# Kernel tuning notes

Hardware: AMD Instinct MI355X
Metric: run time of the kernel (lower is better)

The kernel has to match this reference:

```python
import jax, jax.numpy as jnp
import numpy as np

PATCH = 8
C1 = 1e-4
C2 = 1e-3
EPS = 1e-3
ALPHA = 0.4
WEIGHTS = (1.0, 0.01, 1.0)


def charbonnier(x):
    return (x * x + EPS * EPS) ** ALPHA


def resize_bilinear_ac(img, H2, W2):
    # bilinear resize with align_corners=True (matches F.interpolate)
    B, C, H, W = img.shape
    fy = jnp.arange(H2, dtype=img.dtype) * ((H - 1) / max(H2 - 1, 1))
    fx = jnp.arange(W2, dtype=img.dtype) * ((W - 1) / max(W2 - 1, 1))
    y0 = jnp.clip(jnp.floor(fy).astype(jnp.int32), 0, H - 2)
    x0 = jnp.clip(jnp.floor(fx).astype(jnp.int32), 0, W - 2)
    wy = (fy - y0)[None, None, :, None]
    wx = (fx - x0)[None, None, None, :]
    rows = img[:, :, y0, :] * (1 - wy) + img[:, :, y0 + 1, :] * wy  # [B,C,H2,W]
    out = rows[:, :, :, x0] * (1 - wx) + rows[:, :, :, x0 + 1] * wx  # [B,C,H2,W2]
    return out


def bilinear_warp(img, flow):
    # backward warp: sample img at (x + u, y + v), bilinear, border clamp
    B, C, H, W = img.shape
    gx = jnp.arange(W, dtype=img.dtype)[None, None, :] + flow[:, 0]  # [B,H,W]
    gy = jnp.arange(H, dtype=img.dtype)[None, :, None] + flow[:, 1]  # [B,H,W]
    x0f = jnp.floor(gx)
    y0f = jnp.floor(gy)
    wx = (gx - x0f)[:, None]  # [B,1,H,W]
    wy = (gy - y0f)[:, None]
    x0 = jnp.clip(x0f.astype(jnp.int32), 0, W - 1)
    x1 = jnp.clip(x0 + 1, 0, W - 1)
    y0 = jnp.clip(y0f.astype(jnp.int32), 0, H - 1)
    y1 = jnp.clip(y0 + 1, 0, H - 1)
    imgf = img.reshape(B, C, H * W)

    def gather(yi, xi):
        idx = (yi * W + xi).reshape(B, 1, H * W)
        g = jnp.take_along_axis(imgf, jnp.broadcast_to(idx, (B, C, H * W)), axis=2)
        return g.reshape(B, C, H, W)

    v00 = gather(y0, x0)
    v01 = gather(y0, x1)
    v10 = gather(y1, x0)
    v11 = gather(y1, x1)
    top = v00 * (1 - wx) + v01 * wx
    bot = v10 * (1 - wx) + v11 * wx
    return top * (1 - wy) + bot * wy


def torch_gradient(x, axis):
    # torch.gradient: central diff interior, one-sided at edges, spacing 1
    n = x.shape[axis]
    sl = lambda a, b: jax.lax.slice_in_dim(x, a, b, axis=axis)
    first = sl(1, 2) - sl(0, 1)
    interior = (sl(2, n) - sl(0, n - 2)) * 0.5
    last = sl(n - 1, n) - sl(n - 2, n - 1)
    return jnp.concatenate([first, interior, last], axis=axis)


def ssim_score(I1, I2):
    # faithful to SSIMLoss: stats pooled over ALL non-overlapping patches per
    # (batch, channel), i.e. over the region cropped to multiples of patch.
    B, C, H, W = I1.shape
    p = min(PATCH, H)
    PH, PW = H // p, W // p
    x = I1[:, :, :PH * p, :PW * p].reshape(B, C, -1)
    y = I2[:, :, :PH * p, :PW * p].reshape(B, C, -1)
    N = x.shape[-1]
    mu1 = x.mean(-1)
    mu2 = y.mean(-1)
    d1 = x - mu1[..., None]
    d2 = y - mu2[..., None]
    var1 = (d1 * d1).sum(-1) / (N - 1)  # torch .var() is unbiased
    var2 = (d2 * d2).sum(-1) / (N - 1)
    s12 = (d1 * d2).mean(-1)
    num = (2 * mu1 * mu2 + C1) * (2 * s12 + C2)
    den = (mu1 ** 2 + mu2 ** 2 + C1) * (var1 + var2 + C2)
    return num / den  # [B, C]


def setup_inputs() -> dict:
    key = jax.random.key(0)
    k1, k2 = jax.random.split(key)
    images = jax.random.uniform(k1, (16, 33, 256, 256), dtype=jnp.float32)
    flows = jax.random.normal(k2, (16, 20, 128, 128), dtype=jnp.float32)
    return {"images": images, "flows": flows}


def reference(images, flows):
    B, Cf, FH, FW = flows.shape
    n_flows = Cf // 2  # 10 frame pairs
    imgs = resize_bilinear_ac(images, FH, FW)  # [B,33,FH,FW]
    src = imgs[:, 3:].reshape(B * n_flows, 3, FH, FW)
    fl = flows.reshape(B * n_flows, 2, FH, FW)
    warped = bilinear_warp(src, fl).reshape(B, n_flows * 3, FH, FW)
    ref = imgs[:, : n_flows * 3]

    similarity_loss = ssim_score(ref, warped).mean()

    flow_x = flows[:, 0::2]
    flow_y = flows[:, 1::2]
    smooth = (charbonnier(torch_gradient(flow_x, 1))
              + charbonnier(torch_gradient(flow_x, 2))
              + charbonnier(torch_gradient(flow_y, 1))
              + charbonnier(torch_gradient(flow_y, 2))).mean()

    pixel_loss = charbonnier(ref - warped).mean()

    return WEIGHTS[0] * pixel_loss + WEIGHTS[1] * smooth + WEIGHTS[2] * similarity_loss
```

## Files before the change

kernel.cpp:

```cpp
#include <hip/hip_runtime.h>

#define IH 256
#define IW 256
#define FH 128
#define FW 128
#define NB 16
#define ICH 33
#define NF 10
#define NC 30
#define PL (FH * FW)
#define SPLIT 8
#define ROWS_PP (FH / SPLIT)
#define LOSS_BLOCKS (NB * NC * SPLIT)
#define SMOOTH_BLOCKS 480
#define HALO 5
#define SROWS (ROWS_PP + 2 * HALO + 1)
#define PART_STRIDE 8

__device__ __forceinline__ float charb(float g) {
    float t = fmaf(g, g, 1e-6f);
    return __builtin_amdgcn_exp2f(0.4f * __builtin_amdgcn_logf(t));
}

__device__ __forceinline__ float resized_at(const float* __restrict__ plane, int Y, int X) {
    const float s = (float)(255.0 / 127.0);
    float fy = (float)Y * s;
    float fx = (float)X * s;
    int y0 = (int)fy; y0 = y0 > IH - 2 ? IH - 2 : y0;
    int x0 = (int)fx; x0 = x0 > IW - 2 ? IW - 2 : x0;
    float wy = fy - (float)y0;
    float wx = fx - (float)x0;
    const float* p0 = plane + y0 * IW + x0;
    float v00 = p0[0], v01 = p0[1];
    float v10 = p0[IW], v11 = p0[IW + 1];
    float r0 = v00 * (1.f - wy) + v10 * wy;
    float r1 = v01 * (1.f - wy) + v11 * wy;
    return r0 * (1.f - wx) + r1 * wx;
}

__global__ void __launch_bounds__(256, 8) mega(const float* __restrict__ images,
                                               const float* __restrict__ flows,
                                               float* __restrict__ ws)
{
    float* part_loss   = ws;
    float* part_smooth = ws + LOSS_BLOCKS * PART_STRIDE;

    if (blockIdx.x < SMOOTH_BLOCKS) {
        int sb = blockIdx.x;
        const int total = NB * NF * PL;
        float s = 0.f;
        for (int i = sb * 256 + threadIdx.x; i < total; i += SMOOTH_BLOCKS * 256) {
            int w = i & (FW - 1);
            int h = (i >> 7) & (FH - 1);
            int f = (i >> 14) % NF;
            int b = i / (NF * PL);
            int pix = h * FW + w;
            const float* xp = flows + (size_t)(b * 2 * NF + 2 * f) * PL;
            const float* yp = xp + PL;

            float g1x, g1y;
            if (f == 0)           { g1x = xp[2 * PL + pix] - xp[pix];
                                    g1y = yp[2 * PL + pix] - yp[pix]; }
            else if (f == NF - 1) { g1x = xp[pix] - xp[pix - 2 * PL];
                                    g1y = yp[pix] - yp[pix - 2 * PL]; }
            else                  { g1x = 0.5f * (xp[2 * PL + pix] - xp[pix - 2 * PL]);
                                    g1y = 0.5f * (yp[2 * PL + pix] - yp[pix - 2 * PL]); }

            float g2x, g2y;
            if (h == 0)           { g2x = xp[pix + FW] - xp[pix];
                                    g2y = yp[pix + FW] - yp[pix]; }
            else if (h == FH - 1) { g2x = xp[pix] - xp[pix - FW];
                                    g2y = yp[pix] - yp[pix - FW]; }
            else                  { g2x = 0.5f * (xp[pix + FW] - xp[pix - FW]);
                                    g2y = 0.5f * (yp[pix + FW] - yp[pix - FW]); }

            s += charb(g1x) + charb(g2x) + charb(g1y) + charb(g2y);
        }
        for (int off = 32; off > 0; off >>= 1) s += __shfl_down(s, off, 64);
        __shared__ float shs[4];
        int wave = threadIdx.x >> 6;
        if ((threadIdx.x & 63) == 0) shs[wave] = s;
        __syncthreads();
        if (threadIdx.x == 0)
            part_smooth[sb] = shs[0] + shs[1] + shs[2] + shs[3];
        return;
    }

    __shared__ float slds[SROWS * FW];
    int blk = blockIdx.x - SMOOTH_BLOCKS;
    int bc = blk >> 3;
    int p  = blk & 7;
    int b = bc / NC;
    int c = bc % NC;
    int f = c / 3;
    const float* ref_img  = images + (size_t)(b * ICH + c) * (IH * IW);
    const float* src_img  = images + (size_t)(b * ICH + 3 + c) * (IH * IW);
    const float* fx_plane = flows + (size_t)(b * 2 * NF + 2 * f) * PL;
    const float* fy_plane = fx_plane + PL;

    int lo = p * ROWS_PP - HALO;                    if (lo < 0) lo = 0;
    int hi = p * ROWS_PP + ROWS_PP - 1 + HALO + 1;  if (hi > FH - 1) hi = FH - 1;
    int nstage = (hi - lo + 1) * FW;

    #pragma unroll 2
    for (int i = threadIdx.x; i < nstage; i += 256) {
        int y = lo + (i >> 7);
        int x = i & (FW - 1);
        slds[i] = resized_at(src_img, y, x);
    }
    __syncthreads();

    const float sR = (float)(255.0 / 127.0);
    int w0 = (2 * threadIdx.x) & (FW - 1);
    float fx0 = (float)w0 * sR;
    float fx1 = (float)(w0 + 1) * sR;
    int x00 = (int)fx0; if (x00 > IW - 2) x00 = IW - 2;
    int x01 = (int)fx1; if (x01 > IW - 2) x01 = IW - 2;
    float wxr0 = fx0 - (float)x00;
    float wxr1 = fx1 - (float)x01;

    float s_ref = 0.f, s_w = 0.f, s_r2 = 0.f, s_w2 = 0.f, s_rw = 0.f, s_pix = 0.f;
    int base2 = p * (ROWS_PP * FW / 2);
    for (int i = threadIdx.x; i < ROWS_PP * FW / 2; i += 256) {
        int p2 = base2 + i;
        int px = 2 * p2;
        int h = px >> 7;
        float fyR = (float)h * sR;
        int yr0 = (int)fyR; if (yr0 > IH - 2) yr0 = IH - 2;
        float wyr = fyR - (float)yr0;
        const float* rp0 = ref_img + yr0 * IW;
        const float* rp1 = rp0 + IW;
        float a00 = rp0[x00], a01 = rp0[x00 + 1], a10 = rp1[x00], a11 = rp1[x00 + 1];
        float b00 = rp0[x01], b01 = rp0[x01 + 1], b10 = rp1[x01], b11 = rp1[x01 + 1];
        float2 fl_x = ((const float2*)fx_plane)[p2];
        float2 fl_y = ((const float2*)fy_plane)[p2];

        float ar0 = a00 * (1.f - wyr) + a10 * wyr;
        float ar1 = a01 * (1.f - wyr) + a11 * wyr;
        float ref0 = ar0 * (1.f - wxr0) + ar1 * wxr0;
        float br0 = b00 * (1.f - wyr) + b10 * wyr;
        float br1 = b01 * (1.f - wyr) + b11 * wyr;
        float ref1 = br0 * (1.f - wxr1) + br1 * wxr1;

        float wv[2];
        #pragma unroll
        for (int q = 0; q < 2; q++) {
            float gx = (float)(w0 + q) + (q ? fl_x.y : fl_x.x);
            float gy = (float)h + (q ? fl_y.y : fl_y.x);
            float x0f = floorf(gx), y0f = floorf(gy);
            float wx = gx - x0f, wy = gy - y0f;
            int x0 = (int)x0f; x0 = min(max(x0, 0), FW - 1);
            int y0 = (int)y0f; y0 = min(max(y0, 0), FH - 1);
            int x1 = min(x0 + 1, FW - 1);
            int y1 = min(y0 + 1, FH - 1);
            float v00, v01, v10, v11;
            if (y0 >= lo && y1 <= hi) {
                const float* r0 = slds + ((y0 - lo) << 7);
                const float* r1 = slds + ((y1 - lo) << 7);
                v00 = r0[x0]; v01 = r0[x1];
                v10 = r1[x0]; v11 = r1[x1];
            } else {
                v00 = resized_at(src_img, y0, x0);
                v01 = resized_at(src_img, y0, x1);
                v10 = resized_at(src_img, y1, x0);
                v11 = resized_at(src_img, y1, x1);
            }
            float top = v00 * (1.f - wx) + v01 * wx;
            float bot = v10 * (1.f - wx) + v11 * wx;
            wv[q] = top * (1.f - wy) + bot * wy;
        }

        s_ref += ref0 + ref1;
        s_w   += wv[0] + wv[1];
        s_r2  += ref0 * ref0 + ref1 * ref1;
        s_w2  += wv[0] * wv[0] + wv[1] * wv[1];
        s_rw  += ref0 * wv[0] + ref1 * wv[1];
        s_pix += charb(ref0 - wv[0]) + charb(ref1 - wv[1]);
    }
    for (int off = 32; off > 0; off >>= 1) {
        s_ref += __shfl_down(s_ref, off, 64);
        s_w   += __shfl_down(s_w, off, 64);
        s_r2  += __shfl_down(s_r2, off, 64);
        s_w2  += __shfl_down(s_w2, off, 64);
        s_rw  += __shfl_down(s_rw, off, 64);
        s_pix += __shfl_down(s_pix, off, 64);
    }
    __shared__ float sh[4][6];
    int wave = threadIdx.x >> 6;
    if ((threadIdx.x & 63) == 0) {
        sh[wave][0] = s_ref; sh[wave][1] = s_w; sh[wave][2] = s_r2;
        sh[wave][3] = s_w2;  sh[wave][4] = s_rw; sh[wave][5] = s_pix;
    }
    __syncthreads();
    if (threadIdx.x < 6) {
        int k = threadIdx.x;
        part_loss[blk * PART_STRIDE + k] = sh[0][k] + sh[1][k] + sh[2][k] + sh[3][k];
    }
}

__global__ void __launch_bounds__(512) finalize2(const float* __restrict__ ws,
                                                 float* __restrict__ out)
{
    const float* part_loss   = ws;
    const float* part_smooth = ws + LOSS_BLOCKS * PART_STRIDE;
    int tid = threadIdx.x;
    float ssim = 0.f, pix = 0.f, smo = 0.f;
    if (tid < NB * NC) {
        float t0 = 0, t1 = 0, t2 = 0, t3 = 0, t4 = 0;
        for (int q = 0; q < SPLIT; q++) {
            const float* a = part_loss + (SPLIT * tid + q) * PART_STRIDE;
            t0 += a[0]; t1 += a[1]; t2 += a[2]; t3 += a[3]; t4 += a[4];
            pix += a[5];
        }
        const float N = (float)PL;
        float mu1 = t0 / N, mu2 = t1 / N;
        float var1 = (t2 - t0 * mu1) / (N - 1.f);
        float var2 = (t3 - t1 * mu2) / (N - 1.f);
        float s12 = t4 / N - mu1 * mu2;
        float num = (2.f * mu1 * mu2 + 1e-4f) * (2.f * s12 + 1e-3f);
        float den = (mu1 * mu1 + mu2 * mu2 + 1e-4f) * (var1 + var2 + 1e-3f);
        ssim = num / den;
    }
    if (tid < SMOOTH_BLOCKS) smo = part_smooth[tid];
    __shared__ float sa[512], sb[512], sc[512];
    sa[tid] = ssim; sb[tid] = pix; sc[tid] = smo;
    __syncthreads();
    for (int off = 256; off > 0; off >>= 1) {
        if (tid < off) {
            sa[tid] += sa[tid + off];
            sb[tid] += sb[tid + off];
            sc[tid] += sc[tid + off];
        }
        __syncthreads();
    }
    if (tid == 0) {
        out[0] = sb[0] / (float)(NB * NC * PL)
               + 0.01f * (sc[0] / (float)(NB * NF * PL))
               + sa[0] / (float)(NB * NC);
    }
}

extern "C" void kernel_launch(void* const* d_in, const int* in_sizes, int n_in,
                              void* d_out, int out_size, void* d_ws, size_t ws_size,
                              hipStream_t stream) {
    const float* images = (const float*)d_in[0];
    const float* flows  = (const float*)d_in[1];
    float* ws = (float*)d_ws;
    mega<<<SMOOTH_BLOCKS + LOSS_BLOCKS, 256, 0, stream>>>(images, flows, ws);
    finalize2<<<1, 512, 0, stream>>>(ws, (float*)d_out);
}
```

Baseline: 223.6 us.

## Materialize resized planes in workspace and split loss into separate kernel

Replaces the fused kernel, which resized per block with an LDS halo, with two kernels. The first writes all bilinear-resized planes (33 per batch) to workspace alongside the smoothness reduction. The second computes SSIM and pixel statistics by reading the precomputed ref and src planes, with an XCD-aware block remap and a 4-way split. This removes the redundant resize work spent on halos and on ref recomputation, but adds a round trip through global memory for about 35 MB and an extra kernel launch.

```diff
diff --git a/kernel.cpp b/kernel.cpp
--- a/kernel.cpp
+++ b/kernel.cpp
@@ -9,12 +9,12 @@
 #define NF 10
 #define NC 30
 #define PL (FH * FW)
-#define SPLIT 8
-#define ROWS_PP (FH / SPLIT)
-#define LOSS_BLOCKS (NB * NC * SPLIT)
+#define NPLANE (NB * ICH)
+#define RS_FLOATS (NPLANE * PL)
+#define RSZ_BLOCKS (NPLANE * 4)
 #define SMOOTH_BLOCKS 480
-#define HALO 5
-#define SROWS (ROWS_PP + 2 * HALO + 1)
+#define LOSS_SPLIT 4
+#define LOSS_BLOCKS (NB * NC * LOSS_SPLIT)
 #define PART_STRIDE 8
 
 __device__ __forceinline__ float charb(float g) {
@@ -38,109 +38,97 @@
     return r0 * (1.f - wx) + r1 * wx;
 }
 
-__global__ void __launch_bounds__(256, 8) mega(const float* __restrict__ images,
-                                               const float* __restrict__ flows,
+__global__ void __launch_bounds__(256, 8) resize_smooth(const float* __restrict__ images,
+                                                        const float* __restrict__ flows,
+                                                        float* __restrict__ ws)
+{
+    if (blockIdx.x < RSZ_BLOCKS) {
+        int plane = blockIdx.x >> 2;
+        int quarter = blockIdx.x & 3;
+        const float* img = images + (size_t)plane * (IH * IW);
+        float2* outp = (float2*)ws + (size_t)plane * (PL / 2);
+        #pragma unroll 4
+        for (int k = 0; k < 8; k++) {
+            int p2 = quarter * 2048 + (int)threadIdx.x + k * 256;
+            int Y = p2 >> 6;
+            int X = (p2 & 63) * 2;
+            float r0 = resized_at(img, Y, X);
+            float r1 = resized_at(img, Y, X + 1);
+            outp[p2] = make_float2(r0, r1);
+        }
+        return;
+    }
+
+    float* part_smooth = ws + RS_FLOATS + LOSS_BLOCKS * PART_STRIDE;
+    int sb = blockIdx.x - RSZ_BLOCKS;
+    const int total = NB * NF * PL;
+    float s = 0.f;
+    for (int i = sb * 256 + threadIdx.x; i < total; i += SMOOTH_BLOCKS * 256) {
+        int w = i & (FW - 1);
+        int h = (i >> 7) & (FH - 1);
+        int f = (i >> 14) % NF;
+        int b = i / (NF * PL);
+        int pix = h * FW + w;
+        const float* xp = flows + (size_t)(b * 2 * NF + 2 * f) * PL;
+        const float* yp = xp + PL;
+
+        float g1x, g1y;
+        if (f == 0)           { g1x = xp[2 * PL + pix] - xp[pix];
+                                g1y = yp[2 * PL + pix] - yp[pix]; }
+        else if (f == NF - 1) { g1x = xp[pix] - xp[pix - 2 * PL];
+                                g1y = yp[pix] - yp[pix - 2 * PL]; }
+        else                  { g1x = 0.5f * (xp[2 * PL + pix] - xp[pix - 2 * PL]);
+                                g1y = 0.5f * (yp[2 * PL + pix] - yp[pix - 2 * PL]); }
+
+        float g2x, g2y;
+        if (h == 0)           { g2x = xp[pix + FW] - xp[pix];
+                                g2y = yp[pix + FW] - yp[pix]; }
+        else if (h == FH - 1) { g2x = xp[pix] - xp[pix - FW];
+                                g2y = yp[pix] - yp[pix - FW]; }
+        else                  { g2x = 0.5f * (xp[pix + FW] - xp[pix - FW]);
+                                g2y = 0.5f * (yp[pix + FW] - yp[pix - FW]); }
+
+        s += charb(g1x) + charb(g2x) + charb(g1y) + charb(g2y);
+    }
+    for (int off = 32; off > 0; off >>= 1) s += __shfl_down(s, off, 64);
+    __shared__ float shs[4];
+    int wave = threadIdx.x >> 6;
+    if ((threadIdx.x & 63) == 0) shs[wave] = s;
+    __syncthreads();
+    if (threadIdx.x == 0)
+        part_smooth[sb] = shs[0] + shs[1] + shs[2] + shs[3];
+}
+
+__global__ void __launch_bounds__(256, 8) loss(const float* __restrict__ flows,
                                                float* __restrict__ ws)
 {
-    float* part_loss   = ws;
-    float* part_smooth = ws + LOSS_BLOCKS * PART_STRIDE;
-
-    if (blockIdx.x < SMOOTH_BLOCKS) {
-        int sb = blockIdx.x;
-        const int total = NB * NF * PL;
-        float s = 0.f;
-        for (int i = sb * 256 + threadIdx.x; i < total; i += SMOOTH_BLOCKS * 256) {
-            int w = i & (FW - 1);
-            int h = (i >> 7) & (FH - 1);
-            int f = (i >> 14) % NF;
-            int b = i / (NF * PL);
-            int pix = h * FW + w;
-            const float* xp = flows + (size_t)(b * 2 * NF + 2 * f) * PL;
-            const float* yp = xp + PL;
-
-            float g1x, g1y;
-            if (f == 0)           { g1x = xp[2 * PL + pix] - xp[pix];
-                                    g1y = yp[2 * PL + pix] - yp[pix]; }
-            else if (f == NF - 1) { g1x = xp[pix] - xp[pix - 2 * PL];
-                                    g1y = yp[pix] - yp[pix - 2 * PL]; }
-            else                  { g1x = 0.5f * (xp[2 * PL + pix] - xp[pix - 2 * PL]);
-                                    g1y = 0.5f * (yp[2 * PL + pix] - yp[pix - 2 * PL]); }
-
-            float g2x, g2y;
-            if (h == 0)           { g2x = xp[pix + FW] - xp[pix];
-                                    g2y = yp[pix + FW] - yp[pix]; }
-            else if (h == FH - 1) { g2x = xp[pix] - xp[pix - FW];
-                                    g2y = yp[pix] - yp[pix - FW]; }
-            else                  { g2x = 0.5f * (xp[pix + FW] - xp[pix - FW]);
-                                    g2y = 0.5f * (yp[pix + FW] - yp[pix - FW]); }
-
-            s += charb(g1x) + charb(g2x) + charb(g1y) + charb(g2y);
-        }
-        for (int off = 32; off > 0; off >>= 1) s += __shfl_down(s, off, 64);
-        __shared__ float shs[4];
-        int wave = threadIdx.x >> 6;
-        if ((threadIdx.x & 63) == 0) shs[wave] = s;
-        __syncthreads();
-        if (threadIdx.x == 0)
-            part_smooth[sb] = shs[0] + shs[1] + shs[2] + shs[3];
-        return;
-    }
-
-    __shared__ float slds[SROWS * FW];
-    int blk = blockIdx.x - SMOOTH_BLOCKS;
-    int bc = blk >> 3;
-    int p  = blk & 7;
+    const float* rs = ws;
+    float* part_loss = ws + RS_FLOATS;
+
+    int bid = blockIdx.x;
+    int d = (bid & 7) * (LOSS_BLOCKS / 8) + (bid >> 3);
+    int bc = d >> 2;
+    int part = d & 3;
     int b = bc / NC;
     int c = bc % NC;
     int f = c / 3;
-    const float* ref_img  = images + (size_t)(b * ICH + c) * (IH * IW);
-    const float* src_img  = images + (size_t)(b * ICH + 3 + c) * (IH * IW);
-    const float* fx_plane = flows + (size_t)(b * 2 * NF + 2 * f) * PL;
-    const float* fy_plane = fx_plane + PL;
-
-    int lo = p * ROWS_PP - HALO;                    if (lo < 0) lo = 0;
-    int hi = p * ROWS_PP + ROWS_PP - 1 + HALO + 1;  if (hi > FH - 1) hi = FH - 1;
-    int nstage = (hi - lo + 1) * FW;
-
+    const float2* ref2 = (const float2*)(rs + (size_t)(b * ICH + c) * PL);
+    const float*  src  = rs + (size_t)(b * ICH + 3 + c) * PL;
+    const float2* fx2  = (const float2*)(flows + (size_t)(b * 2 * NF + 2 * f) * PL);
+    const float2* fy2  = (const float2*)(flows + (size_t)(b * 2 * NF + 2 * f + 1) * PL);
+
+    int w0 = (2 * threadIdx.x) & (FW - 1);
+
+    float s_ref = 0.f, s_w = 0.f, s_r2 = 0.f, s_w2 = 0.f, s_rw = 0.f, s_pix = 0.f;
+    int base2 = part * 2048;
     #pragma unroll 2
-    for (int i = threadIdx.x; i < nstage; i += 256) {
-        int y = lo + (i >> 7);
-        int x = i & (FW - 1);
-        slds[i] = resized_at(src_img, y, x);
-    }
-    __syncthreads();
-
-    const float sR = (float)(255.0 / 127.0);
-    int w0 = (2 * threadIdx.x) & (FW - 1);
-    float fx0 = (float)w0 * sR;
-    float fx1 = (float)(w0 + 1) * sR;
-    int x00 = (int)fx0; if (x00 > IW - 2) x00 = IW - 2;
-    int x01 = (int)fx1; if (x01 > IW - 2) x01 = IW - 2;
-    float wxr0 = fx0 - (float)x00;
-    float wxr1 = fx1 - (float)x01;
-
-    float s_ref = 0.f, s_w = 0.f, s_r2 = 0.f, s_w2 = 0.f, s_rw = 0.f, s_pix = 0.f;
-    int base2 = p * (ROWS_PP * FW / 2);
-    for (int i = threadIdx.x; i < ROWS_PP * FW / 2; i += 256) {
-        int p2 = base2 + i;
-        int px = 2 * p2;
-        int h = px >> 7;
-        float fyR = (float)h * sR;
-        int yr0 = (int)fyR; if (yr0 > IH - 2) yr0 = IH - 2;
-        float wyr = fyR - (float)yr0;
-        const float* rp0 = ref_img + yr0 * IW;
-        const float* rp1 = rp0 + IW;
-        float a00 = rp0[x00], a01 = rp0[x00 + 1], a10 = rp1[x00], a11 = rp1[x00 + 1];
-        float b00 = rp0[x01], b01 = rp0[x01 + 1], b10 = rp1[x01], b11 = rp1[x01 + 1];
-        float2 fl_x = ((const float2*)fx_plane)[p2];
-        float2 fl_y = ((const float2*)fy_plane)[p2];
-
-        float ar0 = a00 * (1.f - wyr) + a10 * wyr;
-        float ar1 = a01 * (1.f - wyr) + a11 * wyr;
-        float ref0 = ar0 * (1.f - wxr0) + ar1 * wxr0;
-        float br0 = b00 * (1.f - wyr) + b10 * wyr;
-        float br1 = b01 * (1.f - wyr) + b11 * wyr;
-        float ref1 = br0 * (1.f - wxr1) + br1 * wxr1;
+    for (int k = 0; k < 8; k++) {
+        int p2 = base2 + (int)threadIdx.x + k * 256;
+        int h = p2 >> 6;
+        float2 rv   = ref2[p2];
+        float2 fl_x = fx2[p2];
+        float2 fl_y = fy2[p2];
+        float ref0 = rv.x, ref1 = rv.y;
 
         float wv[2];
         #pragma unroll
@@ -153,18 +141,10 @@
             int y0 = (int)y0f; y0 = min(max(y0, 0), FH - 1);
             int x1 = min(x0 + 1, FW - 1);
             int y1 = min(y0 + 1, FH - 1);
-            float v00, v01, v10, v11;
-            if (y0 >= lo && y1 <= hi) {
-                const float* r0 = slds + ((y0 - lo) << 7);
-                const float* r1 = slds + ((y1 - lo) << 7);
-                v00 = r0[x0]; v01 = r0[x1];
-                v10 = r1[x0]; v11 = r1[x1];
-            } else {
-                v00 = resized_at(src_img, y0, x0);
-                v01 = resized_at(src_img, y0, x1);
-                v10 = resized_at(src_img, y1, x0);
-                v11 = resized_at(src_img, y1, x1);
-            }
+            const float* r0 = src + (y0 << 7);
+            const float* r1 = src + (y1 << 7);
+            float v00 = r0[x0], v01 = r0[x1];
+            float v10 = r1[x0], v11 = r1[x1];
             float top = v00 * (1.f - wx) + v01 * wx;
             float bot = v10 * (1.f - wx) + v11 * wx;
             wv[q] = top * (1.f - wy) + bot * wy;
@@ -193,22 +173,22 @@
     }
     __syncthreads();
     if (threadIdx.x < 6) {
-        int k = threadIdx.x;
-        part_loss[blk * PART_STRIDE + k] = sh[0][k] + sh[1][k] + sh[2][k] + sh[3][k];
+        int j = threadIdx.x;
+        part_loss[d * PART_STRIDE + j] = sh[0][j] + sh[1][j] + sh[2][j] + sh[3][j];
     }
 }
 
 __global__ void __launch_bounds__(512) finalize2(const float* __restrict__ ws,
                                                  float* __restrict__ out)
 {
-    const float* part_loss   = ws;
-    const float* part_smooth = ws + LOSS_BLOCKS * PART_STRIDE;
+    const float* part_loss   = ws + RS_FLOATS;
+    const float* part_smooth = ws + RS_FLOATS + LOSS_BLOCKS * PART_STRIDE;
     int tid = threadIdx.x;
     float ssim = 0.f, pix = 0.f, smo = 0.f;
     if (tid < NB * NC) {
         float t0 = 0, t1 = 0, t2 = 0, t3 = 0, t4 = 0;
-        for (int q = 0; q < SPLIT; q++) {
-            const float* a = part_loss + (SPLIT * tid + q) * PART_STRIDE;
+        for (int q = 0; q < LOSS_SPLIT; q++) {
+            const float* a = part_loss + (LOSS_SPLIT * tid + q) * PART_STRIDE;
             t0 += a[0]; t1 += a[1]; t2 += a[2]; t3 += a[3]; t4 += a[4];
             pix += a[5];
         }
@@ -246,6 +226,7 @@
     const float* images = (const float*)d_in[0];
     const float* flows  = (const float*)d_in[1];
     float* ws = (float*)d_ws;
-    mega<<<SMOOTH_BLOCKS + LOSS_BLOCKS, 256, 0, stream>>>(images, flows, ws);
+    resize_smooth<<<RSZ_BLOCKS + SMOOTH_BLOCKS, 256, 0, stream>>>(images, flows, ws);
+    loss<<<LOSS_BLOCKS, 256, 0, stream>>>(flows, ws);
     finalize2<<<1, 512, 0, stream>>>(ws, (float*)d_out);
 }
```

Measured after the change: 264.4 us. 1.18x slower.
